# Kernel tuning notes

Hardware: AMD Instinct MI355X
Metric: run time of the kernel (lower is better)

## Reference

```python
import jax, jax.numpy as jnp
import numpy as np

N = 100000
IN_C = 128
OUT_C = 200
E = 1600000


def gcn_conv(x, edge_index, W, b):
    """PyG GCNConv: symmetric degree-normalized aggregation with self-loops.
    out[v] = sum_{(u,v) in E+selfloops} d_u^-1/2 d_v^-1/2 (x_u @ W) + b
    """
    n = x.shape[0]
    xw = x @ W  # [N, out]
    loop = jnp.arange(n, dtype=edge_index.dtype)
    row = jnp.concatenate([edge_index[0], loop])  # src
    col = jnp.concatenate([edge_index[1], loop])  # dst
    ones = jnp.ones(row.shape[0], dtype=x.dtype)
    deg = jax.ops.segment_sum(ones, col, num_segments=n)  # in-degree incl. self
    dinv = jnp.where(deg > 0, jax.lax.rsqrt(deg), 0.0)
    norm = dinv[row] * dinv[col]  # [E+N]
    msgs = xw[row] * norm[:, None]  # [E+N, out]
    out = jax.ops.segment_sum(msgs, col, num_segments=n)
    return out + b


def setup_inputs() -> dict:
    key = jax.random.key(0)
    k1, k2, k3, k4 = jax.random.split(key, 4)
    x = jax.random.normal(k1, (N, IN_C), dtype=jnp.float32)
    edge_index = jax.random.randint(k2, (2, E), 0, N, dtype=jnp.int64)
    s1 = 1.0 / np.sqrt(IN_C)
    W1 = jax.random.uniform(k3, (IN_C, OUT_C), dtype=jnp.float32, minval=-s1, maxval=s1)
    b1 = jnp.zeros((OUT_C,), dtype=jnp.float32)
    W2 = jax.random.uniform(k4, (IN_C, OUT_C), dtype=jnp.float32, minval=-s1, maxval=s1)
    b2 = jnp.zeros((OUT_C,), dtype=jnp.float32)
    return {"x": x, "edge_index": edge_index, "W1": W1, "b1": b1, "W2": W2, "b2": b2}


def reference(x, edge_index, W1, b1, W2, b2):
    mu = gcn_conv(x, edge_index, W1, b1)
    logstd = gcn_conv(x, edge_index, W2, b2)
    return (mu, logstd)
```

## Files before the change

### kernel.cpp

```cpp
#include <hip/hip_runtime.h>

#define N_NODES 100000
#define IN_C    128
#define OUT_C   200
#define NT_TILES 13
#define KT_TILES 4

#define PSHIFT  8
#define NPB     256
#define NB      391
#define NB_POW2 512
#define BCAP    5120
#define PART_CH 8192

typedef __bf16 bf16_t;
typedef bf16_t bf16x8 __attribute__((ext_vector_type(8)));
typedef float  f32x4  __attribute__((ext_vector_type(4)));

__device__ __forceinline__ unsigned int bf16_bits(float f) {
    unsigned int u = __builtin_bit_cast(unsigned int, f);
    return (u + 0x7FFFu + ((u >> 16) & 1u)) >> 16;
}
__device__ __forceinline__ float bf16_lo(unsigned int p) {
    return __builtin_bit_cast(float, p << 16);
}
__device__ __forceinline__ float bf16_hi(unsigned int p) {
    return __builtin_bit_cast(float, p & 0xFFFF0000u);
}

__global__ __launch_bounds__(256) void partition_kernel(
        const int* __restrict__ row, const int* __restrict__ col, int E,
        int* __restrict__ gcount, unsigned int* __restrict__ gbuf) {
    __shared__ int hist[NB];
    __shared__ int base[NB];
    __shared__ int lofs[NB];
    __shared__ int pscan[256];
    __shared__ unsigned int stage[PART_CH];
    __shared__ unsigned short sb[PART_CH];
    const int tid = threadIdx.x;
    const int chunk = blockIdx.x * PART_CH;
    int cend = E - chunk; if (cend > PART_CH) cend = PART_CH;

    for (int i = tid; i < NB; i += 256) hist[i] = 0;
    __syncthreads();

    for (int i = tid; i < cend; i += 256) {
        int b = (col[chunk + i] >> PSHIFT) & (NB_POW2 - 1);
        if (b >= NB) b = NB - 1;
        atomicAdd(&hist[b], 1);
    }
    __syncthreads();

    for (int i = tid; i < NB; i += 256)
        base[i] = atomicAdd(&gcount[i], hist[i]);

    int v0 = (2 * tid     < NB) ? hist[2 * tid]     : 0;
    int v1 = (2 * tid + 1 < NB) ? hist[2 * tid + 1] : 0;
    int s = v0 + v1;
    pscan[tid] = s;
    __syncthreads();
    for (int off = 1; off < 256; off <<= 1) {
        int u = (tid >= off) ? pscan[tid - off] : 0;
        __syncthreads();
        pscan[tid] += u;
        __syncthreads();
    }
    int ep = pscan[tid] - s;
    if (2 * tid     < NB) lofs[2 * tid]     = ep;
    if (2 * tid + 1 < NB) lofs[2 * tid + 1] = ep + v0;
    __syncthreads();

    for (int i = tid; i < NB; i += 256) hist[i] = 0;
    __syncthreads();
    for (int i = tid; i < cend; i += 256) {
        int c = col[chunk + i];
        int r = row[chunk + i];
        int b = (c >> PSHIFT) & (NB_POW2 - 1);
        if (b >= NB) b = NB - 1;
        int p = lofs[b] + atomicAdd(&hist[b], 1);
        stage[p] = (unsigned int)((c & (NPB - 1)) | (r << PSHIFT));
        sb[p] = (unsigned short)b;
    }
    __syncthreads();

    for (int i = tid; i < cend; i += 256) {
        int b = sb[i];
        int p = base[b] + (i - lofs[b]);
        if (p < BCAP) gbuf[(size_t)b * BCAP + p] = stage[i];
    }
}

__global__ void bucket_scan_kernel(const int* __restrict__ gcount, int* __restrict__ gbase) {
    __shared__ int pscan[256];
    int tid = threadIdx.x;
    int v0 = (2 * tid     < NB) ? gcount[2 * tid]     : 0;
    int v1 = (2 * tid + 1 < NB) ? gcount[2 * tid + 1] : 0;
    if (v0 > BCAP) v0 = BCAP;
    if (v1 > BCAP) v1 = BCAP;
    int s = v0 + v1;
    pscan[tid] = s;
    __syncthreads();
    for (int off = 1; off < 256; off <<= 1) {
        int u = (tid >= off) ? pscan[tid - off] : 0;
        __syncthreads();
        pscan[tid] += u;
        __syncthreads();
    }
    int ep = pscan[tid] - s;
    if (2 * tid     < NB) gbase[2 * tid]     = ep;
    if (2 * tid + 1 < NB) gbase[2 * tid + 1] = ep + v0;
}

__global__ __launch_bounds__(256) void build_kernel(
        const unsigned int* __restrict__ gbuf, const int* __restrict__ gcount,
        const int* __restrict__ gbase, int* __restrict__ deg,
        int* __restrict__ offsets, int* __restrict__ csr_src, int n) {
    __shared__ int cnt[NPB];
    __shared__ int cur[NPB];
    __shared__ int pscan[256];
    const int b = blockIdx.x;
    const int tid = threadIdx.x;
    int total = gcount[b]; if (total > BCAP) total = BCAP;
    const int cbase = gbase[b];
    const unsigned int* bp = gbuf + (size_t)b * BCAP;

    cnt[tid] = 0;
    __syncthreads();
    for (int i = tid; i < total; i += 256)
        atomicAdd(&cnt[bp[i] & (NPB - 1)], 1);
    __syncthreads();

    int c = cnt[tid];
    pscan[tid] = c;
    __syncthreads();
    for (int off = 1; off < 256; off <<= 1) {
        int u = (tid >= off) ? pscan[tid - off] : 0;
        __syncthreads();
        pscan[tid] += u;
        __syncthreads();
    }
    int excl = pscan[tid] - c;
    cur[tid] = excl;
    int v = b * NPB + tid;
    if (v < n) { deg[v] = c; offsets[v] = cbase + excl; }
    __syncthreads();

    for (int i = tid; i < total; i += 256) {
        unsigned int e = bp[i];
        int p = atomicAdd(&cur[e & (NPB - 1)], 1);
        csr_src[cbase + p] = (int)(e >> PSHIFT);
    }
}

__global__ void dinv_kernel(const int* __restrict__ deg, float* __restrict__ dinv, int n) {
    int v = blockIdx.x * blockDim.x + threadIdx.x;
    if (v < n) dinv[v] = rsqrtf((float)(deg[v] + 1));
}

__global__ void convert_xs_kernel(const float* __restrict__ x, const float* __restrict__ dinv,
                                  unsigned int* __restrict__ xs2, int n) {
    int id = blockIdx.x * blockDim.x + threadIdx.x;
    if (id >= n * 64) return;
    int v = id >> 6;
    float dv = dinv[v];
    float2 f = ((const float2*)x)[id];
    unsigned int lo = bf16_bits(f.x * dv);
    unsigned int hi = bf16_bits(f.y * dv);
    xs2[id] = lo | (hi << 16);
}

__global__ __launch_bounds__(256) void gather_kernel(
        const unsigned int* __restrict__ xs2, const float* __restrict__ dinv,
        const int* __restrict__ offsets, const int* __restrict__ deg,
        const int* __restrict__ csr_src, unsigned int* __restrict__ agg2, int n) {
    int wave = threadIdx.x >> 6;
    int lane = threadIdx.x & 63;
    int v = blockIdx.x * 4 + wave;
    if (v >= n) return;
    float dv = dinv[v];
    int start = offsets[v];
    int cnt = deg[v];
    unsigned int s = xs2[(size_t)v * 64 + lane];
    float ax = bf16_lo(s), ay = bf16_hi(s);

    const int* cp = csr_src + start;
    int i = 0;
    for (; i + 8 <= cnt; i += 8) {
        int u[8];
        #pragma unroll
        for (int j = 0; j < 8; j++) u[j] = cp[i + j];
        unsigned int t[8];
        #pragma unroll
        for (int j = 0; j < 8; j++) t[j] = xs2[(size_t)u[j] * 64 + lane];
        #pragma unroll
        for (int j = 0; j < 8; j++) { ax += bf16_lo(t[j]); ay += bf16_hi(t[j]); }
    }
    if (i + 4 <= cnt) {
        int u[4];
        #pragma unroll
        for (int j = 0; j < 4; j++) u[j] = cp[i + j];
        unsigned int t[4];
        #pragma unroll
        for (int j = 0; j < 4; j++) t[j] = xs2[(size_t)u[j] * 64 + lane];
        #pragma unroll
        for (int j = 0; j < 4; j++) { ax += bf16_lo(t[j]); ay += bf16_hi(t[j]); }
        i += 4;
    }
    for (; i < cnt; i++) {
        int u = cp[i];
        unsigned int t = xs2[(size_t)u * 64 + lane];
        ax += bf16_lo(t); ay += bf16_hi(t);
    }
    ax *= dv; ay *= dv;
    agg2[(size_t)v * 64 + lane] = bf16_bits(ax) | (bf16_bits(ay) << 16);
}

__global__ void pack_w_kernel(const float* __restrict__ W1, const float* __restrict__ W2,
                              unsigned short* __restrict__ out) {
    int tid = blockIdx.x * blockDim.x + threadIdx.x;
    if (tid >= 2 * KT_TILES * NT_TILES * 64) return;
    int lane = tid & 63;
    int nt = (tid >> 6) % NT_TILES;
    int kt = (tid / (64 * NT_TILES)) % KT_TILES;
    int h  = tid / (64 * NT_TILES * KT_TILES);
    const float* W = h ? W2 : W1;
    int q = lane >> 4, r = lane & 15;
    int nn = nt * 16 + r;
    size_t dst = ((size_t)((nt * 2 + h) * KT_TILES + kt)) * 512 + (size_t)lane * 8;
    for (int j = 0; j < 8; j++) {
        int k = kt * 32 + q * 8 + j;
        float val = (nn < OUT_C) ? W[(size_t)k * OUT_C + nn] : 0.f;
        out[dst + j] = (unsigned short)bf16_bits(val);
    }
}

__global__ __launch_bounds__(256) void gemm_mfma_kernel(
        const unsigned short* __restrict__ agg,
        const unsigned short* __restrict__ Wpk,
        const float* __restrict__ b1, const float* __restrict__ b2,
        float* __restrict__ mu, float* __restrict__ ls, int M) {
    __shared__ uint4 Bs[2][512];
    int tid  = threadIdx.x;
    int wave = tid >> 6;
    int lane = tid & 63;
    int row0 = blockIdx.x * 64 + wave * 16;
    int q = lane >> 4, r = lane & 15;

    int arow = row0 + r; if (arow > M - 1) arow = M - 1;
    const unsigned short* ap = agg + (size_t)arow * IN_C + q * 8;
    bf16x8 afrag[KT_TILES];
    #pragma unroll
    for (int kt = 0; kt < KT_TILES; kt++) {
        uint4 u = *(const uint4*)(ap + kt * 32);
        afrag[kt] = __builtin_bit_cast(bf16x8, u);
    }

    f32x4 acc[2][NT_TILES];
    #pragma unroll
    for (int h = 0; h < 2; h++)
        #pragma unroll
        for (int nt = 0; nt < NT_TILES; nt++)
            acc[h][nt] = (f32x4){0.f, 0.f, 0.f, 0.f};

    const uint4* wsrc = (const uint4*)Wpk;
    uint4 pre0 = wsrc[tid];
    uint4 pre1 = wsrc[tid + 256];

    for (int nt = 0; nt < NT_TILES; nt++) {
        int buf = nt & 1;
        Bs[buf][tid]       = pre0;
        Bs[buf][tid + 256] = pre1;
        __syncthreads();
        if (nt + 1 < NT_TILES) {
            pre0 = wsrc[(nt + 1) * 512 + tid];
            pre1 = wsrc[(nt + 1) * 512 + tid + 256];
        }
        #pragma unroll
        for (int h = 0; h < 2; h++) {
            f32x4 c = acc[h][nt];
            #pragma unroll
            for (int kt = 0; kt < KT_TILES; kt++) {
                uint4 u = Bs[buf][(h * KT_TILES + kt) * 64 + lane];
                bf16x8 bfrag = __builtin_bit_cast(bf16x8, u);
                c = __builtin_amdgcn_mfma_f32_16x16x32_bf16(afrag[kt], bfrag, c, 0, 0, 0);
            }
            acc[h][nt] = c;
        }
    }

    #pragma unroll
    for (int nt = 0; nt < NT_TILES; nt++) {
        int col = nt * 16 + r;
        bool cok = col < OUT_C;
        float bv1 = cok ? b1[col] : 0.f;
        float bv2 = cok ? b2[col] : 0.f;
        #pragma unroll
        for (int reg = 0; reg < 4; reg++) {
            int gr = row0 + q * 4 + reg;
            if (cok && gr < M) {
                mu[(size_t)gr * OUT_C + col] = acc[0][nt][reg] + bv1;
                ls[(size_t)gr * OUT_C + col] = acc[1][nt][reg] + bv2;
            }
        }
    }
}

extern "C" void kernel_launch(void* const* d_in, const int* in_sizes, int n_in,
                              void* d_out, int out_size, void* d_ws, size_t ws_size,
                              hipStream_t stream) {
    const float* x  = (const float*)d_in[0];
    const int*   ei = (const int*)d_in[1];
    const float* W1 = (const float*)d_in[2];
    const float* b1 = (const float*)d_in[3];
    const float* W2 = (const float*)d_in[4];
    const float* b2 = (const float*)d_in[5];

    const int n = in_sizes[0] / IN_C;
    const int E = in_sizes[1] / 2;
    const int* row = ei;
    const int* col = ei + E;

    float* mu = (float*)d_out;
    float* ls = (float*)d_out + (size_t)n * OUT_C;

    char* ws = (char*)d_ws;
    int*            deg     = (int*)           (ws + 0);
    float*          dinv    = (float*)         (ws + 524288);
    int*            offsets = (int*)           (ws + 1048576);
    int*            gcount  = (int*)           (ws + 1572864);
    int*            gbase   = (int*)           (ws + 1576960);
    int*            csr_src = (int*)           (ws + 2162688);
    unsigned int*   xs2     = (unsigned int*)  (ws + 8562688);
    unsigned int*   gbuf    = (unsigned int*)  (ws + 34162688);
    unsigned int*   agg2    = (unsigned int*)  (ws + 34162688);
    unsigned short* Wpk     = (unsigned short*)(ws + 59762688);

    hipMemsetAsync(gcount, 0, NB * sizeof(int), stream);

    pack_w_kernel<<<(2 * KT_TILES * NT_TILES * 64 + 255) / 256, 256, 0, stream>>>(W1, W2, Wpk);

    partition_kernel<<<(E + PART_CH - 1) / PART_CH, 256, 0, stream>>>(row, col, E, gcount, gbuf);
    bucket_scan_kernel<<<1, 256, 0, stream>>>(gcount, gbase);
    build_kernel<<<NB, 256, 0, stream>>>(gbuf, gcount, gbase, deg, offsets, csr_src, n);

    dinv_kernel<<<(n + 255) / 256, 256, 0, stream>>>(deg, dinv, n);
    convert_xs_kernel<<<(n * 64 + 255) / 256, 256, 0, stream>>>(x, dinv, xs2, n);

    gather_kernel<<<(n + 3) / 4, 256, 0, stream>>>(xs2, dinv, offsets, deg, csr_src, agg2, n);

    gemm_mfma_kernel<<<(n + 63) / 64, 256, 0, stream>>>(
        (const unsigned short*)agg2, Wpk, b1, b2, mu, ls, n);
}
```

Baseline: 423.3 us.

## Fuse neighbor gather into MFMA GEMM and fold dinv into CSR build

New measurement: 467.5 us. 1.1x slower.

```diff
diff --git a/kernel.cpp b/kernel.cpp
--- a/kernel.cpp
+++ b/kernel.cpp
@@ -114,7 +114,8 @@
 __global__ __launch_bounds__(256) void build_kernel(
         const unsigned int* __restrict__ gbuf, const int* __restrict__ gcount,
         const int* __restrict__ gbase, int* __restrict__ deg,
-        int* __restrict__ offsets, int* __restrict__ csr_src, int n) {
+        int* __restrict__ offsets, float* __restrict__ dinv,
+        int* __restrict__ csr_src, int n) {
     __shared__ int cnt[NPB];
     __shared__ int cur[NPB];
     __shared__ int pscan[256];
@@ -142,7 +143,11 @@
     int excl = pscan[tid] - c;
     cur[tid] = excl;
     int v = b * NPB + tid;
-    if (v < n) { deg[v] = c; offsets[v] = cbase + excl; }
+    if (v < n) {
+        deg[v] = c;
+        offsets[v] = cbase + excl;
+        dinv[v] = rsqrtf((float)(c + 1));
+    }
     __syncthreads();
 
     for (int i = tid; i < total; i += 256) {
@@ -152,67 +157,17 @@
     }
 }
 
-__global__ void dinv_kernel(const int* __restrict__ deg, float* __restrict__ dinv, int n) {
-    int v = blockIdx.x * blockDim.x + threadIdx.x;
-    if (v < n) dinv[v] = rsqrtf((float)(deg[v] + 1));
-}
-
-__global__ void convert_xs_kernel(const float* __restrict__ x, const float* __restrict__ dinv,
-                                  unsigned int* __restrict__ xs2, int n) {
+__global__ void convert_xs_kernel(const float4* __restrict__ x, const float* __restrict__ dinv,
+                                  uint2* __restrict__ xs4, int n) {
     int id = blockIdx.x * blockDim.x + threadIdx.x;
-    if (id >= n * 64) return;
-    int v = id >> 6;
+    if (id >= n * 32) return;
+    int v = id >> 5;
     float dv = dinv[v];
-    float2 f = ((const float2*)x)[id];
-    unsigned int lo = bf16_bits(f.x * dv);
-    unsigned int hi = bf16_bits(f.y * dv);
-    xs2[id] = lo | (hi << 16);
-}
-
-__global__ __launch_bounds__(256) void gather_kernel(
-        const unsigned int* __restrict__ xs2, const float* __restrict__ dinv,
-        const int* __restrict__ offsets, const int* __restrict__ deg,
-        const int* __restrict__ csr_src, unsigned int* __restrict__ agg2, int n) {
-    int wave = threadIdx.x >> 6;
-    int lane = threadIdx.x & 63;
-    int v = blockIdx.x * 4 + wave;
-    if (v >= n) return;
-    float dv = dinv[v];
-    int start = offsets[v];
-    int cnt = deg[v];
-    unsigned int s = xs2[(size_t)v * 64 + lane];
-    float ax = bf16_lo(s), ay = bf16_hi(s);
-
-    const int* cp = csr_src + start;
-    int i = 0;
-    for (; i + 8 <= cnt; i += 8) {
-        int u[8];
-        #pragma unroll
-        for (int j = 0; j < 8; j++) u[j] = cp[i + j];
-        unsigned int t[8];
-        #pragma unroll
-        for (int j = 0; j < 8; j++) t[j] = xs2[(size_t)u[j] * 64 + lane];
-        #pragma unroll
-        for (int j = 0; j < 8; j++) { ax += bf16_lo(t[j]); ay += bf16_hi(t[j]); }
-    }
-    if (i + 4 <= cnt) {
-        int u[4];
-        #pragma unroll
-        for (int j = 0; j < 4; j++) u[j] = cp[i + j];
-        unsigned int t[4];
-        #pragma unroll
-        for (int j = 0; j < 4; j++) t[j] = xs2[(size_t)u[j] * 64 + lane];
-        #pragma unroll
-        for (int j = 0; j < 4; j++) { ax += bf16_lo(t[j]); ay += bf16_hi(t[j]); }
-        i += 4;
-    }
-    for (; i < cnt; i++) {
-        int u = cp[i];
-        unsigned int t = xs2[(size_t)u * 64 + lane];
-        ax += bf16_lo(t); ay += bf16_hi(t);
-    }
-    ax *= dv; ay *= dv;
-    agg2[(size_t)v * 64 + lane] = bf16_bits(ax) | (bf16_bits(ay) << 16);
+    float4 f = x[id];
+    uint2 o;
+    o.x = bf16_bits(f.x * dv) | (bf16_bits(f.y * dv) << 16);
+    o.y = bf16_bits(f.z * dv) | (bf16_bits(f.w * dv) << 16);
+    xs4[id] = o;
 }
 
 __global__ void pack_w_kernel(const float* __restrict__ W1, const float* __restrict__ W2,
@@ -234,11 +189,14 @@
     }
 }
 
-__global__ __launch_bounds__(256) void gemm_mfma_kernel(
-        const unsigned short* __restrict__ agg,
+__global__ __launch_bounds__(256) void fused_gather_gemm_kernel(
+        const unsigned int* __restrict__ xs2, const float* __restrict__ dinv,
+        const int* __restrict__ offsets, const int* __restrict__ deg,
+        const int* __restrict__ csr_src,
         const unsigned short* __restrict__ Wpk,
         const float* __restrict__ b1, const float* __restrict__ b2,
         float* __restrict__ mu, float* __restrict__ ls, int M) {
+    __shared__ unsigned int Astripe[4][16][64];
     __shared__ uint4 Bs[2][512];
     int tid  = threadIdx.x;
     int wave = tid >> 6;
@@ -246,12 +204,56 @@
     int row0 = blockIdx.x * 64 + wave * 16;
     int q = lane >> 4, r = lane & 15;
 
-    int arow = row0 + r; if (arow > M - 1) arow = M - 1;
-    const unsigned short* ap = agg + (size_t)arow * IN_C + q * 8;
+    const uint4* wsrc = (const uint4*)Wpk;
+    uint4 pre0 = wsrc[tid];
+    uint4 pre1 = wsrc[tid + 256];
+
+    for (int m = 0; m < 16; m++) {
+        int v = row0 + m;
+        if (v >= M) { Astripe[wave][m][lane] = 0; continue; }
+        float dv = dinv[v];
+        int start = offsets[v];
+        int cnt = deg[v];
+        unsigned int s = xs2[(size_t)v * 64 + lane];
+        float ax = bf16_lo(s), ay = bf16_hi(s);
+
+        const int* cp = csr_src + start;
+        int i = 0;
+        for (; i + 8 <= cnt; i += 8) {
+            int u[8];
+            #pragma unroll
+            for (int j = 0; j < 8; j++) u[j] = cp[i + j];
+            unsigned int t[8];
+            #pragma unroll
+            for (int j = 0; j < 8; j++) t[j] = xs2[(size_t)u[j] * 64 + lane];
+            #pragma unroll
+            for (int j = 0; j < 8; j++) { ax += bf16_lo(t[j]); ay += bf16_hi(t[j]); }
+        }
+        if (i + 4 <= cnt) {
+            int u[4];
+            #pragma unroll
+            for (int j = 0; j < 4; j++) u[j] = cp[i + j];
+            unsigned int t[4];
+            #pragma unroll
+            for (int j = 0; j < 4; j++) t[j] = xs2[(size_t)u[j] * 64 + lane];
+            #pragma unroll
+            for (int j = 0; j < 4; j++) { ax += bf16_lo(t[j]); ay += bf16_hi(t[j]); }
+            i += 4;
+        }
+        for (; i < cnt; i++) {
+            int u = cp[i];
+            unsigned int t = xs2[(size_t)u * 64 + lane];
+            ax += bf16_lo(t); ay += bf16_hi(t);
+        }
+        ax *= dv; ay *= dv;
+        Astripe[wave][m][lane] = bf16_bits(ax) | (bf16_bits(ay) << 16);
+    }
+
+    const unsigned int* as = &Astripe[wave][r][0];
     bf16x8 afrag[KT_TILES];
     #pragma unroll
     for (int kt = 0; kt < KT_TILES; kt++) {
-        uint4 u = *(const uint4*)(ap + kt * 32);
+        uint4 u = *(const uint4*)(as + kt * 16 + q * 4);
         afrag[kt] = __builtin_bit_cast(bf16x8, u);
     }
 
@@ -261,10 +263,6 @@
         #pragma unroll
         for (int nt = 0; nt < NT_TILES; nt++)
             acc[h][nt] = (f32x4){0.f, 0.f, 0.f, 0.f};
-
-    const uint4* wsrc = (const uint4*)Wpk;
-    uint4 pre0 = wsrc[tid];
-    uint4 pre1 = wsrc[tid + 256];
 
     for (int nt = 0; nt < NT_TILES; nt++) {
         int buf = nt & 1;
@@ -332,7 +330,6 @@
     int*            csr_src = (int*)           (ws + 2162688);
     unsigned int*   xs2     = (unsigned int*)  (ws + 8562688);
     unsigned int*   gbuf    = (unsigned int*)  (ws + 34162688);
-    unsigned int*   agg2    = (unsigned int*)  (ws + 34162688);
     unsigned short* Wpk     = (unsigned short*)(ws + 59762688);
 
     hipMemsetAsync(gcount, 0, NB * sizeof(int), stream);
@@ -341,13 +338,11 @@
 
     partition_kernel<<<(E + PART_CH - 1) / PART_CH, 256, 0, stream>>>(row, col, E, gcount, gbuf);
     bucket_scan_kernel<<<1, 256, 0, stream>>>(gcount, gbase);
-    build_kernel<<<NB, 256, 0, stream>>>(gbuf, gcount, gbase, deg, offsets, csr_src, n);
-
-    dinv_kernel<<<(n + 255) / 256, 256, 0, stream>>>(deg, dinv, n);
-    convert_xs_kernel<<<(n * 64 + 255) / 256, 256, 0, stream>>>(x, dinv, xs2, n);
-
-    gather_kernel<<<(n + 3) / 4, 256, 0, stream>>>(xs2, dinv, offsets, deg, csr_src, agg2, n);
-
-    gemm_mfma_kernel<<<(n + 63) / 64, 256, 0, stream>>>(
-        (const unsigned short*)agg2, Wpk, b1, b2, mu, ls, n);
-}
+    build_kernel<<<NB, 256, 0, stream>>>(gbuf, gcount, gbase, deg, offsets, dinv, csr_src, n);
+
+    convert_xs_kernel<<<(n * 32 + 255) / 256, 256, 0, stream>>>(
+        (const float4*)x, dinv, (uint2*)xs2, n);
+
+    fused_gather_gemm_kernel<<<(n + 63) / 64, 256, 0, stream>>>(
+        xs2, dinv, offsets, deg, csr_src, Wpk, b1, b2, mu, ls, n);
+}
```
